# Kernel optimization log

Measured on AMD Instinct MI355X. Metric: run time of the kernel, lower is better.

Reference implementation:

```python
import jax, jax.numpy as jnp
import numpy as np

N, E_RAND, IN, HID, OUT = 10000, 320000, 512, 256, 256
E = E_RAND + N  # random edges + self loops
TEMP, LAM, LAMBDA_LOSS, BN_EPS = 0.5, 1e-3, 1.0, 1e-5


def _normalize(x):
    # F.normalize: x / max(||x||, 1e-12)
    return x / jnp.maximum(jnp.linalg.norm(x, axis=-1, keepdims=True), 1e-12)


def setup_inputs() -> dict:
    key = jax.random.key(0)
    ks = jax.random.split(key, 12)
    feat = jax.random.normal(ks[0], (N, IN), jnp.float32)
    loops = jnp.arange(N)
    src = jnp.concatenate([jax.random.randint(ks[1], (E_RAND,), 0, N), loops])
    dst = jnp.concatenate([jax.random.randint(ks[2], (E_RAND,), 0, N), loops])
    def lin(k, i, o):
        return jax.random.normal(k, (i, o), jnp.float32) / np.sqrt(i).astype(np.float32)
    return {
        'feat': feat,
        'W1': lin(ks[3], IN, HID), 'b1': jnp.zeros((HID,), jnp.float32),
        'W2': lin(ks[4], HID, OUT), 'b2': jnp.zeros((OUT,), jnp.float32),
        'Wt1': lin(ks[5], IN, HID), 'bt1': jnp.zeros((HID,), jnp.float32),
        'gamma': jnp.ones((HID,), jnp.float32), 'beta': jnp.zeros((HID,), jnp.float32),
        'Wt2': lin(ks[6], HID, OUT), 'bt2': jnp.zeros((OUT,), jnp.float32),
        'Wp': lin(ks[7], HID, HID), 'bp': jnp.zeros((HID,), jnp.float32),
        'src': src, 'dst': dst,
    }


def reference(feat, W1, b1, W2, b2, Wt1, bt1, gamma, beta, Wt2, bt2, Wp, bp, src, dst):
    n = feat.shape[0]
    ones = jnp.ones(src.shape, feat.dtype)
    deg_out = jax.ops.segment_sum(ones, src, num_segments=n)
    deg_in = jax.ops.segment_sum(ones, dst, num_segments=n)
    # symmetric GCN norm per edge (self-loops included so degrees >= 1)
    norm_e = jax.lax.rsqrt(deg_out)[src] * jax.lax.rsqrt(deg_in)[dst]

    def gconv(x, W, b):
        xw = x @ W  # [n, d_out]
        agg = jax.ops.segment_sum(xw[src] * norm_e[:, None], dst, num_segments=n)
        return agg + b

    # GCN encoder (2 layers, no LN)
    h = jax.nn.relu(gconv(feat, W1, b1))
    h = gconv(h, W2, b2)

    # target MLP encoder: linear -> BN(train) -> relu -> linear
    t = feat @ Wt1 + bt1
    mu = t.mean(0)
    var = t.var(0)  # biased, as BatchNorm normalization
    t = (t - mu) * jax.lax.rsqrt(var + BN_EPS) * gamma + beta
    trans = jax.nn.relu(t) @ Wt2 + bt2

    z = _normalize(h)                    # [n, d]
    q = _normalize(trans @ Wp + bp)      # projector (num_MLP=1)

    # pos_score: per-edge sum(z[u]*q[v])/temp, mean over in-edges at v
    sim_e = jnp.einsum('ed,ed->e', z[src], q[dst]) / TEMP
    pos = jax.ops.segment_sum(sim_e, dst, num_segments=n) / deg_in

    # neg_score (neg_sample=0): dense NxN similarity row-sums
    neg_sim = jnp.exp(z @ z.T / TEMP).sum(1)           # per-node
    neg_sim2 = LAM * jnp.exp(z @ q.T / TEMP).sum(1)    # per-node
    m_e = jnp.log(neg_sim[dst] + neg_sim2[src])
    neg = jax.ops.segment_sum(m_e, dst, num_segments=n) / deg_in

    loss = jnp.mean(-pos + LAMBDA_LOSS * neg)
    return loss
```

## Files before the change

### kernel.cpp

```cpp
#include <hip/hip_runtime.h>
#include <stdint.h>


#define TEMP_INV 2.0f
#define LAMC 1.0e-3f
#define SSCALE 1.6986436f

typedef __attribute__((ext_vector_type(8))) __bf16 bf16x8;
typedef __attribute__((ext_vector_type(4))) float f32x4;

__device__ __forceinline__ unsigned short f2bf(float x) {
  union { float f; unsigned int u; } v; v.f = x;
  unsigned int r = v.u + 0x7FFFu + ((v.u >> 16) & 1u);
  return (unsigned short)(r >> 16);
}

__device__ __forceinline__ void g2lds16(const void* gc, void* l) {
  void* g = const_cast<void*>(gc);
  __builtin_amdgcn_global_load_lds(
      (__attribute__((address_space(1))) void*)g,
      (__attribute__((address_space(3))) void*)l, 16, 0, 0);
}

__global__ void k_deg(const int* __restrict__ src, const int* __restrict__ dst,
                      float* deg_out, float* deg_in, int E) {
  int i = blockIdx.x * blockDim.x + threadIdx.x;
  if (i < E) {
    atomicAdd(&deg_out[src[i]], 1.0f);
    atomicAdd(&deg_in[dst[i]], 1.0f);
  }
}

__global__ void k_rdeg(const float* __restrict__ deg_out, const float* __restrict__ deg_in,
                       float* rdo, float* rdi, float* idi, int N) {
  int i = blockIdx.x * blockDim.x + threadIdx.x;
  if (i < N) {
    float o = deg_out[i], d = deg_in[i];
    rdo[i] = rsqrtf(o);
    rdi[i] = rsqrtf(d);
    idi[i] = 1.0f / d;
  }
}

__global__ void k_scan(const float* __restrict__ deg, int* __restrict__ off, int N, int E) {
  __shared__ int sm[1024];
  int tid = threadIdx.x;
  int chunk = (N + 1023) / 1024;
  int b = tid * chunk;
  int sum = 0;
  for (int j = 0; j < chunk; j++) { int i = b + j; if (i < N) sum += (int)deg[i]; }
  sm[tid] = sum;
  __syncthreads();
  for (int s = 1; s < 1024; s <<= 1) {
    int v = (tid >= s) ? sm[tid - s] : 0;
    __syncthreads();
    sm[tid] += v;
    __syncthreads();
  }
  int run = (tid == 0) ? 0 : sm[tid - 1];
  for (int j = 0; j < chunk; j++) {
    int i = b + j;
    if (i < N) { off[i] = run; run += (int)deg[i]; }
  }
  if (tid == 0) off[N] = E;
}

__global__ void k_fill(const int* __restrict__ src, const int* __restrict__ dst,
                       const int* __restrict__ off, int* cur,
                       const float* __restrict__ rdo, const float* __restrict__ rdi,
                       int* adj, float* aw, int E) {
  int e = blockIdx.x * blockDim.x + threadIdx.x;
  if (e < E) {
    int u = src[e], v = dst[e];
    int slot = off[v] + atomicAdd(&cur[v], 1);
    adj[slot] = u;
    aw[slot] = rdo[u] * rdi[v];
  }
}

template <int K, bool BIAS>
__global__ __launch_bounds__(256, 2) void k_gemm(const float* A, const float* __restrict__ W,
                                                 const float* __restrict__ bias, float* C, int M) {
  __shared__ float At[32][68];
  __shared__ float Wl[32][256];
  int tid = threadIdx.x;
  int rg = tid >> 4, cg = tid & 15;
  int r0 = rg * 4, cb = cg * 4;
  int row0 = blockIdx.x * 64;
  float acc[4][16] = {};
  for (int k0 = 0; k0 < K; k0 += 32) {
    __syncthreads();
#pragma unroll
    for (int t = 0; t < 2; t++) {
      int lin = tid + 256 * t;
      int r = lin >> 3, k4 = (lin & 7) * 4;
      int ar = row0 + r; if (ar >= M) ar = M - 1;
      float4 a4 = *(const float4*)(A + (size_t)ar * K + k0 + k4);
      At[k4 + 0][r] = a4.x; At[k4 + 1][r] = a4.y;
      At[k4 + 2][r] = a4.z; At[k4 + 3][r] = a4.w;
    }
#pragma unroll
    for (int t = 0; t < 8; t++) {
      int lin = tid + 256 * t;
      int kk = lin >> 6, c4 = (lin & 63) * 4;
      *(float4*)&Wl[kk][c4] = *(const float4*)(W + (size_t)(k0 + kk) * 256 + c4);
    }
    __syncthreads();
#pragma unroll
    for (int k = 0; k < 32; k++) {
      float4 a4 = *(const float4*)&At[k][r0];
      float av[4] = {a4.x, a4.y, a4.z, a4.w};
#pragma unroll
      for (int t = 0; t < 4; t++) {
        float4 w4 = *(const float4*)&Wl[k][64 * t + cb];
#pragma unroll
        for (int i = 0; i < 4; i++) {
          acc[i][4 * t + 0] += av[i] * w4.x;
          acc[i][4 * t + 1] += av[i] * w4.y;
          acc[i][4 * t + 2] += av[i] * w4.z;
          acc[i][4 * t + 3] += av[i] * w4.w;
        }
      }
    }
  }
#pragma unroll
  for (int i = 0; i < 4; i++) {
    int r = row0 + r0 + i;
    if (r < M) {
      float* crow = C + (size_t)r * 256;
#pragma unroll
      for (int t = 0; t < 4; t++) {
        int c = 64 * t + cb;
        float4 v = {acc[i][4 * t], acc[i][4 * t + 1], acc[i][4 * t + 2], acc[i][4 * t + 3]};
        if constexpr (BIAS) {
          float4 b4 = *(const float4*)(bias + c);
          v.x += b4.x; v.y += b4.y; v.z += b4.z; v.w += b4.w;
        }
        *(float4*)(crow + c) = v;
      }
    }
  }
}

__global__ void k_bnstat(const float* __restrict__ T, float* s, float* ss, int M) {
  int c = threadIdx.x;
  int r0 = blockIdx.x * 64;
  float a = 0, b = 0;
  for (int r = r0; r < r0 + 64 && r < M; r++) {
    float v = T[(size_t)r * 256 + c];
    a += v; b += v * v;
  }
  atomicAdd(&s[c], a);
  atomicAdd(&ss[c], b);
}

__global__ void k_bnrelu(float* T, const float* __restrict__ s, const float* __restrict__ ss,
                         const float* __restrict__ g, const float* __restrict__ b, int M) {
  int r = blockIdx.x, c = threadIdx.x;
  float invM = 1.0f / (float)M;
  float mu = s[c] * invM;
  float var = ss[c] * invM - mu * mu;
  float w = rsqrtf(var + 1e-5f) * g[c];
  float v = T[(size_t)r * 256 + c];
  v = (v - mu) * w + b[c];
  T[(size_t)r * 256 + c] = fmaxf(v, 0.0f);
}

template <bool UNIT, bool RELU>
__global__ __launch_bounds__(256) void k_agg(const float* __restrict__ X, const int* __restrict__ off,
                                             const int* __restrict__ adj, const float* __restrict__ w,
                                             const float* __restrict__ bias, float* __restrict__ Y, int N) {
  int wv = threadIdx.x >> 6, ln = threadIdx.x & 63;
  int v = blockIdx.x * 4 + wv;
  if (v >= N) return;
  int s0 = off[v], s1 = off[v + 1];
  const float4* X4 = (const float4*)X;
  float4 acc = {0, 0, 0, 0};
  for (int s = s0; s < s1; s++) {
    int u = adj[s];
    float wt = UNIT ? 1.0f : w[s];
    float4 x = X4[(size_t)u * 64 + ln];
    acc.x += wt * x.x; acc.y += wt * x.y; acc.z += wt * x.z; acc.w += wt * x.w;
  }
  if constexpr (!UNIT) {
    float4 b = ((const float4*)bias)[ln];
    acc.x += b.x; acc.y += b.y; acc.z += b.z; acc.w += b.w;
  }
  if constexpr (RELU) {
    acc.x = fmaxf(acc.x, 0.f); acc.y = fmaxf(acc.y, 0.f);
    acc.z = fmaxf(acc.z, 0.f); acc.w = fmaxf(acc.w, 0.f);
  }
  ((float4*)Y)[(size_t)v * 64 + ln] = acc;
}

__global__ __launch_bounds__(256) void k_norm(float* X, unsigned short* Xb, int N, int NPAD) {
  int wv = threadIdx.x >> 6, ln = threadIdx.x & 63;
  int r = blockIdx.x * 4 + wv;
  if (r >= NPAD) return;
  if (r >= N) {
    ushort4 z = {0, 0, 0, 0};
    ((ushort4*)Xb)[(size_t)r * 64 + ln] = z;
    return;
  }
  float4 x = ((const float4*)X)[(size_t)r * 64 + ln];
  float ss = x.x * x.x + x.y * x.y + x.z * x.z + x.w * x.w;
#pragma unroll
  for (int m = 1; m < 64; m <<= 1) ss += __shfl_xor(ss, m, 64);
  float sc = 1.0f / fmaxf(sqrtf(ss), 1e-12f);
  float4 xn = {x.x * sc, x.y * sc, x.z * sc, x.w * sc};
  ((float4*)X)[(size_t)r * 64 + ln] = xn;
  float bs = sc * SSCALE;
  ushort4 b;
  b.x = f2bf(x.x * bs); b.y = f2bf(x.y * bs);
  b.z = f2bf(x.z * bs); b.w = f2bf(x.w * bs);
  ((ushort4*)Xb)[(size_t)r * 64 + ln] = b;
}

__global__ __launch_bounds__(256, 2) void k_sim(const unsigned short* __restrict__ Zb,
                                                const unsigned short* __restrict__ Qb,
                                                float* __restrict__ S1, float* __restrict__ S2,
                                                int N, int JT, int JS) {
  __shared__ __align__(1024) char LB[65536];
  const int tid = threadIdx.x;
  const int wv = tid >> 6, ln = tid & 63;
  const int i0 = blockIdx.x * 128;

#pragma unroll
  for (int it = 0; it < 16; it++) {
    int c = it * 4 + wv;
    int L = c * 1024 + ln * 16;
    int r = L >> 9;
    int o = (L & 511) ^ ((r & 7) << 4);
    g2lds16((const char*)Zb + (size_t)(i0 + r) * 512 + o, (char*)LB + c * 1024);
  }
  __syncthreads();

  bf16x8 af[2][8];
#pragma unroll
  for (int rf = 0; rf < 2; rf++) {
    int lrow = wv * 32 + rf * 16 + (ln & 15);
#pragma unroll
    for (int kk = 0; kk < 8; kk++) {
      int o = (kk * 64 + ((ln >> 4) << 4)) ^ ((lrow & 7) << 4);
      af[rf][kk] = *(const bf16x8*)(LB + lrow * 512 + o);
    }
  }

  f32x4 rs[2][2] = {};

  int jt0 = (blockIdx.y * JT) / JS;
  int jt1 = ((blockIdx.y + 1) * JT) / JS;
  for (int jt = jt0; jt < jt1; jt++) {
    int j0 = jt * 64;
    __syncthreads();
#pragma unroll
    for (int it = 0; it < 16; it++) {
      int c = it * 4 + wv;
      int L = c * 1024 + ln * 16;
      int r = L >> 9;
      int o = (L & 511) ^ ((r & 7) << 4);
      const char* base = (r < 64) ? (const char*)Zb + (size_t)(j0 + r) * 512
                                  : (const char*)Qb + (size_t)(j0 + r - 64) * 512;
      g2lds16(base + o, (char*)LB + c * 1024);
    }
    __syncthreads();

    f32x4 accZ[2][4] = {};
    f32x4 accQ[2][4] = {};
#pragma unroll
    for (int cf = 0; cf < 4; cf++) {
      int brow = cf * 16 + (ln & 15);
#pragma unroll
      for (int kk = 0; kk < 8; kk++) {
        int o = (kk * 64 + ((ln >> 4) << 4)) ^ ((brow & 7) << 4);
        bf16x8 bz = *(const bf16x8*)(LB + brow * 512 + o);
        bf16x8 bq = *(const bf16x8*)(LB + (brow + 64) * 512 + o);
        accZ[0][cf] = __builtin_amdgcn_mfma_f32_16x16x32_bf16(af[0][kk], bz, accZ[0][cf], 0, 0, 0);
        accZ[1][cf] = __builtin_amdgcn_mfma_f32_16x16x32_bf16(af[1][kk], bz, accZ[1][cf], 0, 0, 0);
        accQ[0][cf] = __builtin_amdgcn_mfma_f32_16x16x32_bf16(af[0][kk], bq, accQ[0][cf], 0, 0, 0);
        accQ[1][cf] = __builtin_amdgcn_mfma_f32_16x16x32_bf16(af[1][kk], bq, accQ[1][cf], 0, 0, 0);
      }
    }
#pragma unroll
    for (int rf = 0; rf < 2; rf++)
#pragma unroll
      for (int cf = 0; cf < 4; cf++)
#pragma unroll
        for (int i = 0; i < 4; i++) {
          rs[rf][0][i] += exp2f(accZ[rf][cf][i]);
          rs[rf][1][i] += exp2f(accQ[rf][cf][i]);
        }
  }

#pragma unroll
  for (int rf = 0; rf < 2; rf++)
#pragma unroll
    for (int m = 0; m < 2; m++)
#pragma unroll
      for (int i = 0; i < 4; i++) {
        float v = rs[rf][m][i];
        v += __shfl_xor(v, 1, 64);
        v += __shfl_xor(v, 2, 64);
        v += __shfl_xor(v, 4, 64);
        v += __shfl_xor(v, 8, 64);
        if ((ln & 15) == 0) {
          int row = i0 + wv * 32 + rf * 16 + ((ln >> 4) << 2) + i;
          if (row < N) atomicAdd(((m == 0) ? S1 : S2) + row, v);
        }
      }
}

__global__ __launch_bounds__(256) void k_final(const float* __restrict__ zsum, const float* __restrict__ q,
                                               const float* __restrict__ S1, const float* __restrict__ S2,
                                               const int* __restrict__ off, const int* __restrict__ adj,
                                               const float* __restrict__ idi, float* __restrict__ out,
                                               int N, float pad) {
  int wv = threadIdx.x >> 6, ln = threadIdx.x & 63;
  int v = blockIdx.x * 4 + wv;
  if (v >= N) return;
  float4 zs = ((const float4*)zsum)[(size_t)v * 64 + ln];
  float4 qv = ((const float4*)q)[(size_t)v * 64 + ln];
  float d = zs.x * qv.x + zs.y * qv.y + zs.z * qv.z + zs.w * qv.w;
  float s1v = S1[v] - pad;
  float lg = 0.0f;
  int e0 = off[v], e1 = off[v + 1];
  for (int s = e0 + ln; s < e1; s += 64) {
    int u = adj[s];
    lg += logf(s1v + LAMC * (S2[u] - pad));
  }
#pragma unroll
  for (int m = 1; m < 64; m <<= 1) {
    d += __shfl_xor(d, m, 64);
    lg += __shfl_xor(lg, m, 64);
  }
  if (ln == 0) {
    float inv = idi[v];
    float posv = d * inv * TEMP_INV;
    float negv = lg * inv;
    atomicAdd(out, (negv - posv) * (1.0f / (float)N));
  }
}

extern "C" void kernel_launch(void* const* d_in, const int* in_sizes, int n_in,
                              void* d_out, int out_size, void* d_ws, size_t ws_size,
                              hipStream_t stream) {
  const float* feat  = (const float*)d_in[0];
  const float* W1    = (const float*)d_in[1];
  const float* b1    = (const float*)d_in[2];
  const float* W2    = (const float*)d_in[3];
  const float* b2    = (const float*)d_in[4];
  const float* Wt1   = (const float*)d_in[5];
  const float* bt1   = (const float*)d_in[6];
  const float* gamma = (const float*)d_in[7];
  const float* beta  = (const float*)d_in[8];
  const float* Wt2   = (const float*)d_in[9];
  const float* bt2   = (const float*)d_in[10];
  const float* Wp    = (const float*)d_in[11];
  const float* bp    = (const float*)d_in[12];
  const int*   src   = (const int*)d_in[13];
  const int*   dst   = (const int*)d_in[14];
  const int N = in_sizes[0] / 512;
  const int E = in_sizes[13];
  const int NTI = (N + 127) / 128, NPAD = NTI * 128, JT = NPAD / 64;
  const int JS = 13;
  const float PADF = (float)(NPAD - N);

  char* p = (char*)d_ws;
  auto alloc = [&](size_t bytes) { char* r = p; p += (bytes + 255) & ~(size_t)255; return r; };
  float* B0 = (float*)alloc((size_t)N * 256 * 4);
  float* B1 = (float*)alloc((size_t)N * 256 * 4);
  float* B2 = (float*)alloc((size_t)N * 256 * 4);
  unsigned short* zb = (unsigned short*)alloc((size_t)NPAD * 256 * 2);
  unsigned short* qb = (unsigned short*)alloc((size_t)NPAD * 256 * 2);
  int*   off = (int*)alloc((size_t)(N + 1) * 4);
  int*   adj = (int*)alloc((size_t)E * 4);
  float* aw  = (float*)alloc((size_t)E * 4);
  char*  zblk = p;
  float* deg_out = (float*)alloc((size_t)N * 4);
  float* deg_in  = (float*)alloc((size_t)N * 4);
  int*   cur     = (int*)alloc((size_t)N * 4);
  float* S1 = (float*)alloc((size_t)N * 4);
  float* S2 = (float*)alloc((size_t)N * 4);
  float* bns  = (float*)alloc(256 * 4);
  float* bnss = (float*)alloc(256 * 4);
  size_t zbytes = (size_t)(p - zblk);
  float* rdo = (float*)alloc((size_t)N * 4);
  float* rdi = (float*)alloc((size_t)N * 4);
  float* idi = (float*)alloc((size_t)N * 4);
  (void)ws_size; (void)n_in; (void)out_size;

  hipMemsetAsync(zblk, 0, zbytes, stream);
  hipMemsetAsync(d_out, 0, 4, stream);

  int gE = (E + 255) / 256, gN = (N + 255) / 256, gb = (N + 63) / 64, gw = (N + 3) / 4;
  k_deg<<<gE, 256, 0, stream>>>(src, dst, deg_out, deg_in, E);
  k_rdeg<<<gN, 256, 0, stream>>>(deg_out, deg_in, rdo, rdi, idi, N);
  k_scan<<<1, 1024, 0, stream>>>(deg_in, off, N, E);
  k_fill<<<gE, 256, 0, stream>>>(src, dst, off, cur, rdo, rdi, adj, aw, E);

  k_gemm<512, false><<<gb, 256, 0, stream>>>(feat, W1, nullptr, B0, N);
  k_gemm<512, true ><<<gb, 256, 0, stream>>>(feat, Wt1, bt1, B1, N);
  k_bnstat<<<(N + 63) / 64, 256, 0, stream>>>(B1, bns, bnss, N);
  k_bnrelu<<<N, 256, 0, stream>>>(B1, bns, bnss, gamma, beta, N);
  k_gemm<256, true ><<<gb, 256, 0, stream>>>(B1, Wt2, bt2, B1, N);
  k_gemm<256, true ><<<gb, 256, 0, stream>>>(B1, Wp, bp, B1, N);

  k_agg<false, true ><<<gw, 256, 0, stream>>>(B0, off, adj, aw, b1, B2, N);
  k_gemm<256, false><<<gb, 256, 0, stream>>>(B2, W2, nullptr, B0, N);
  k_agg<false, false><<<gw, 256, 0, stream>>>(B0, off, adj, aw, b2, B2, N);

  int gnp = (NPAD + 3) / 4;
  k_norm<<<gnp, 256, 0, stream>>>(B2, zb, N, NPAD);
  k_norm<<<gnp, 256, 0, stream>>>(B1, qb, N, NPAD);

  dim3 gs(NTI, JS);
  k_sim<<<gs, 256, 0, stream>>>(zb, qb, S1, S2, N, JT, JS);

  k_agg<true, false><<<gw, 256, 0, stream>>>(B2, off, adj, aw, nullptr, B0, N);
  k_final<<<gw, 256, 0, stream>>>(B0, B1, S1, S2, off, adj, idi, (float*)d_out, N, PADF);
}
```

Before: 881.8 us.

## Double-buffer the similarity kernel with larger row tiles and fuse the two feat GEMMs

The dense similarity kernel now gives each block 256 rows (64 per wave) of Z held in registers, loaded straight from global memory. It double-buffers 32-row Z/Q column tiles in LDS so the next tile's load overlaps the current tile's MFMAs. The grid split and padding change to match (NPAD multiple of 256, JS 25). Separately, the two GEMMs that both read feat (W1 and Wt1) are merged into one kernel, so feat is read once. The merged kernel carries two accumulator sets per thread, which raises register pressure and may lower occupancy.

Result: no change. 884.4 us (+0.3%).

```diff
diff --git a/kernel.cpp b/kernel.cpp
--- a/kernel.cpp
+++ b/kernel.cpp
@@ -137,6 +137,75 @@
           v.x += b4.x; v.y += b4.y; v.z += b4.z; v.w += b4.w;
         }
         *(float4*)(crow + c) = v;
+      }
+    }
+  }
+}
+
+__global__ __launch_bounds__(256, 2) void k_gemm2(const float* __restrict__ A,
+                                                  const float* __restrict__ W1f,
+                                                  const float* __restrict__ W2f,
+                                                  const float* __restrict__ b2f,
+                                                  float* __restrict__ C1, float* __restrict__ C2,
+                                                  int M) {
+  __shared__ float At[32][68];
+  __shared__ float Wl[2][32][256];
+  int tid = threadIdx.x;
+  int rg = tid >> 4, cg = tid & 15;
+  int r0 = rg * 4, cb = cg * 4;
+  int row0 = blockIdx.x * 64;
+  float acc1[4][16] = {};
+  float acc2[4][16] = {};
+  for (int k0 = 0; k0 < 512; k0 += 32) {
+    __syncthreads();
+#pragma unroll
+    for (int t = 0; t < 2; t++) {
+      int lin = tid + 256 * t;
+      int r = lin >> 3, k4 = (lin & 7) * 4;
+      int ar = row0 + r; if (ar >= M) ar = M - 1;
+      float4 a4 = *(const float4*)(A + (size_t)ar * 512 + k0 + k4);
+      At[k4 + 0][r] = a4.x; At[k4 + 1][r] = a4.y;
+      At[k4 + 2][r] = a4.z; At[k4 + 3][r] = a4.w;
+    }
+#pragma unroll
+    for (int t = 0; t < 8; t++) {
+      int lin = tid + 256 * t;
+      int kk = lin >> 6, c4 = (lin & 63) * 4;
+      *(float4*)&Wl[0][kk][c4] = *(const float4*)(W1f + (size_t)(k0 + kk) * 256 + c4);
+      *(float4*)&Wl[1][kk][c4] = *(const float4*)(W2f + (size_t)(k0 + kk) * 256 + c4);
+    }
+    __syncthreads();
+#pragma unroll
+    for (int k = 0; k < 32; k++) {
+      float4 a4 = *(const float4*)&At[k][r0];
+      float av[4] = {a4.x, a4.y, a4.z, a4.w};
+#pragma unroll
+      for (int t = 0; t < 4; t++) {
+        float4 w4 = *(const float4*)&Wl[0][k][64 * t + cb];
+        float4 u4 = *(const float4*)&Wl[1][k][64 * t + cb];
+#pragma unroll
+        for (int i = 0; i < 4; i++) {
+          acc1[i][4 * t + 0] += av[i] * w4.x; acc1[i][4 * t + 1] += av[i] * w4.y;
+          acc1[i][4 * t + 2] += av[i] * w4.z; acc1[i][4 * t + 3] += av[i] * w4.w;
+          acc2[i][4 * t + 0] += av[i] * u4.x; acc2[i][4 * t + 1] += av[i] * u4.y;
+          acc2[i][4 * t + 2] += av[i] * u4.z; acc2[i][4 * t + 3] += av[i] * u4.w;
+        }
+      }
+    }
+  }
+#pragma unroll
+  for (int i = 0; i < 4; i++) {
+    int r = row0 + r0 + i;
+    if (r < M) {
+#pragma unroll
+      for (int t = 0; t < 4; t++) {
+        int c = 64 * t + cb;
+        float4 v1 = {acc1[i][4 * t], acc1[i][4 * t + 1], acc1[i][4 * t + 2], acc1[i][4 * t + 3]};
+        float4 v2 = {acc2[i][4 * t], acc2[i][4 * t + 1], acc2[i][4 * t + 2], acc2[i][4 * t + 3]};
+        float4 b4 = *(const float4*)(b2f + c);
+        v2.x += b4.x; v2.y += b4.y; v2.z += b4.z; v2.w += b4.w;
+        *(float4*)(C1 + (size_t)r * 256 + c) = v1;
+        *(float4*)(C2 + (size_t)r * 256 + c) = v2;
       }
     }
   }
@@ -220,80 +289,75 @@
                                                 const unsigned short* __restrict__ Qb,
                                                 float* __restrict__ S1, float* __restrict__ S2,
                                                 int N, int JT, int JS) {
-  __shared__ __align__(1024) char LB[65536];
+  __shared__ __align__(1024) char LB[2][32768];
   const int tid = threadIdx.x;
   const int wv = tid >> 6, ln = tid & 63;
-  const int i0 = blockIdx.x * 128;
-
-#pragma unroll
-  for (int it = 0; it < 16; it++) {
-    int c = it * 4 + wv;
-    int L = c * 1024 + ln * 16;
-    int r = L >> 9;
-    int o = (L & 511) ^ ((r & 7) << 4);
-    g2lds16((const char*)Zb + (size_t)(i0 + r) * 512 + o, (char*)LB + c * 1024);
-  }
-  __syncthreads();
-
-  bf16x8 af[2][8];
-#pragma unroll
-  for (int rf = 0; rf < 2; rf++) {
-    int lrow = wv * 32 + rf * 16 + (ln & 15);
-#pragma unroll
-    for (int kk = 0; kk < 8; kk++) {
-      int o = (kk * 64 + ((ln >> 4) << 4)) ^ ((lrow & 7) << 4);
-      af[rf][kk] = *(const bf16x8*)(LB + lrow * 512 + o);
-    }
-  }
-
-  f32x4 rs[2][2] = {};
-
-  int jt0 = (blockIdx.y * JT) / JS;
-  int jt1 = ((blockIdx.y + 1) * JT) / JS;
-  for (int jt = jt0; jt < jt1; jt++) {
-    int j0 = jt * 64;
-    __syncthreads();
-#pragma unroll
-    for (int it = 0; it < 16; it++) {
+  const int i0 = blockIdx.x * 256;
+  const int wb = wv * 64;
+
+  auto STAGE = [&](int jt, int b) {
+    int j0 = jt * 32;
+    char* Lb = (char*)LB[b];
+#pragma unroll
+    for (int it = 0; it < 8; it++) {
       int c = it * 4 + wv;
       int L = c * 1024 + ln * 16;
       int r = L >> 9;
       int o = (L & 511) ^ ((r & 7) << 4);
-      const char* base = (r < 64) ? (const char*)Zb + (size_t)(j0 + r) * 512
-                                  : (const char*)Qb + (size_t)(j0 + r - 64) * 512;
-      g2lds16(base + o, (char*)LB + c * 1024);
-    }
-    __syncthreads();
-
-    f32x4 accZ[2][4] = {};
-    f32x4 accQ[2][4] = {};
-#pragma unroll
-    for (int cf = 0; cf < 4; cf++) {
-      int brow = cf * 16 + (ln & 15);
+      const char* g = (r < 32) ? (const char*)Zb + (size_t)(j0 + r) * 512 + o
+                               : (const char*)Qb + (size_t)(j0 + r - 32) * 512 + o;
+      g2lds16(g, Lb + c * 1024);
+    }
+  };
+
+  int jt0 = (blockIdx.y * JT) / JS;
+  int jt1 = ((blockIdx.y + 1) * JT) / JS;
+
+  STAGE(jt0, 0);
+
+  bf16x8 af[4][8];
+#pragma unroll
+  for (int rf = 0; rf < 4; rf++) {
+    const char* arow = (const char*)(Zb + (size_t)(i0 + wb + rf * 16 + (ln & 15)) * 256);
+#pragma unroll
+    for (int kk = 0; kk < 8; kk++)
+      af[rf][kk] = *(const bf16x8*)(arow + kk * 64 + ((ln >> 4) << 4));
+  }
+
+  f32x4 rs[4][2] = {};
+
+  __syncthreads();
+  int cur = 0;
+  for (int jt = jt0; jt < jt1; jt++) {
+    if (jt + 1 < jt1) STAGE(jt + 1, cur ^ 1);
+    const char* Lb = (const char*)LB[cur];
+#pragma unroll
+    for (int m = 0; m < 2; m++) {
+      f32x4 acc[4][2] = {};
 #pragma unroll
       for (int kk = 0; kk < 8; kk++) {
-        int o = (kk * 64 + ((ln >> 4) << 4)) ^ ((brow & 7) << 4);
-        bf16x8 bz = *(const bf16x8*)(LB + brow * 512 + o);
-        bf16x8 bq = *(const bf16x8*)(LB + (brow + 64) * 512 + o);
-        accZ[0][cf] = __builtin_amdgcn_mfma_f32_16x16x32_bf16(af[0][kk], bz, accZ[0][cf], 0, 0, 0);
-        accZ[1][cf] = __builtin_amdgcn_mfma_f32_16x16x32_bf16(af[1][kk], bz, accZ[1][cf], 0, 0, 0);
-        accQ[0][cf] = __builtin_amdgcn_mfma_f32_16x16x32_bf16(af[0][kk], bq, accQ[0][cf], 0, 0, 0);
-        accQ[1][cf] = __builtin_amdgcn_mfma_f32_16x16x32_bf16(af[1][kk], bq, accQ[1][cf], 0, 0, 0);
-      }
-    }
-#pragma unroll
-    for (int rf = 0; rf < 2; rf++)
-#pragma unroll
-      for (int cf = 0; cf < 4; cf++)
-#pragma unroll
-        for (int i = 0; i < 4; i++) {
-          rs[rf][0][i] += exp2f(accZ[rf][cf][i]);
-          rs[rf][1][i] += exp2f(accQ[rf][cf][i]);
+#pragma unroll
+        for (int cf = 0; cf < 2; cf++) {
+          int brow = m * 32 + cf * 16 + (ln & 15);
+          int o = (kk * 64 + ((ln >> 4) << 4)) ^ ((brow & 7) << 4);
+          bf16x8 bb = *(const bf16x8*)(Lb + brow * 512 + o);
+#pragma unroll
+          for (int rf = 0; rf < 4; rf++)
+            acc[rf][cf] = __builtin_amdgcn_mfma_f32_16x16x32_bf16(af[rf][kk], bb, acc[rf][cf], 0, 0, 0);
         }
-  }
-
-#pragma unroll
-  for (int rf = 0; rf < 2; rf++)
+      }
+#pragma unroll
+      for (int rf = 0; rf < 4; rf++)
+#pragma unroll
+        for (int i = 0; i < 4; i++)
+          rs[rf][m][i] += exp2f(acc[rf][0][i]) + exp2f(acc[rf][1][i]);
+    }
+    __syncthreads();
+    cur ^= 1;
+  }
+
+#pragma unroll
+  for (int rf = 0; rf < 4; rf++)
 #pragma unroll
     for (int m = 0; m < 2; m++)
 #pragma unroll
@@ -304,7 +368,7 @@
         v += __shfl_xor(v, 4, 64);
         v += __shfl_xor(v, 8, 64);
         if ((ln & 15) == 0) {
-          int row = i0 + wv * 32 + rf * 16 + ((ln >> 4) << 2) + i;
+          int row = i0 + wb + rf * 16 + ((ln >> 4) << 2) + i;
           if (row < N) atomicAdd(((m == 0) ? S1 : S2) + row, v);
         }
       }
@@ -361,8 +425,8 @@
   const int*   dst   = (const int*)d_in[14];
   const int N = in_sizes[0] / 512;
   const int E = in_sizes[13];
-  const int NTI = (N + 127) / 128, NPAD = NTI * 128, JT = NPAD / 64;
-  const int JS = 13;
+  const int NTI = (N + 255) / 256, NPAD = NTI * 256, JT = NPAD / 32;
+  const int JS = 25;
   const float PADF = (float)(NPAD - N);
 
   char* p = (char*)d_ws;
@@ -398,8 +462,7 @@
   k_scan<<<1, 1024, 0, stream>>>(deg_in, off, N, E);
   k_fill<<<gE, 256, 0, stream>>>(src, dst, off, cur, rdo, rdi, adj, aw, E);
 
-  k_gemm<512, false><<<gb, 256, 0, stream>>>(feat, W1, nullptr, B0, N);
-  k_gemm<512, true ><<<gb, 256, 0, stream>>>(feat, Wt1, bt1, B1, N);
+  k_gemm2<<<gb, 256, 0, stream>>>(feat, W1, Wt1, bt1, B0, B1, N);
   k_bnstat<<<(N + 63) / 64, 256, 0, stream>>>(B1, bns, bnss, N);
   k_bnrelu<<<N, 256, 0, stream>>>(B1, bns, bnss, gamma, beta, N);
   k_gemm<256, true ><<<gb, 256, 0, stream>>>(B1, Wt2, bt2, B1, N);
```
